# Kernel optimization log

Measured on AMD Instinct MI355X. Metric: run time of the kernel, lower is better.

## Reference

```python
import jax, jax.numpy as jnp
import numpy as np

# DenseCRFParams defaults (kernel bandwidths chosen O(1) since points ~ N(0,1))
GAMMA = 1.0   # spatial kernel bandwidth
ALPHA = 1.0   # bilateral spatial bandwidth
BETA = 1.0    # bilateral feature bandwidth
SPATIAL_KER_WEIGHT = 3.0
BILATERAL_KER_WEIGHT = 5.0
NUM_LABELS = 13
NUM_ITERATIONS = 5
N_POINTS = 8192


def _gauss_kernel(feats):
    # K_ij = exp(-0.5 * ||f_i - f_j||^2), feats: (n, d) -> (n, n)
    sq = jnp.sum(feats * feats, axis=-1)
    d2 = sq[:, None] + sq[None, :] - 2.0 * (feats @ feats.T)
    return jnp.exp(-0.5 * jnp.maximum(d2, 0.0))


def setup_inputs() -> dict:
    key = jax.random.key(0)
    k1, k2 = jax.random.split(key)
    points = jax.random.normal(k1, (N_POINTS, 6), dtype=jnp.float32)
    logits = jax.random.normal(k2, (N_POINTS, NUM_LABELS), dtype=jnp.float32)
    eye = jnp.eye(NUM_LABELS, dtype=jnp.float32)
    return {
        "points": points,
        "logits": logits,
        "spatial_ker_weights": SPATIAL_KER_WEIGHT * eye,
        "bilateral_ker_weights": BILATERAL_KER_WEIGHT * eye,
        "compatibility_matrix": eye,
    }


def reference(points, logits, spatial_ker_weights, bilateral_ker_weights, compatibility_matrix):
    n, num_labels = logits.shape
    xyz = points[:, :3]
    feat = points[:, 3:]

    # Exact Gaussian filtering (the math the permutohedral lattice approximates),
    # normalized by the filter response to all-ones (splat-blur-slice normalization).
    k_spatial = _gauss_kernel(xyz / GAMMA)                                   # (n, n)
    k_bilateral = _gauss_kernel(jnp.concatenate([xyz / ALPHA, feat / BETA], axis=-1))
    norm_s = jnp.sum(k_spatial, axis=1, keepdims=True)                       # (n, 1)
    norm_b = jnp.sum(k_bilateral, axis=1, keepdims=True)

    cur_logits = logits
    for _ in range(NUM_ITERATIONS):
        # NOTE: original uses Softmax(dim=0), i.e. over the point axis — kept faithful.
        q = jax.nn.softmax(cur_logits, axis=0)                               # (n, L)
        spatial_filt = (k_spatial @ q) / norm_s                              # (n, L)
        bilateral_filt = (k_bilateral @ q) / norm_b                          # (n, L)
        # NOTE: original does .view(num_labels, -1) — a raw row-major reshape,
        # NOT a transpose; replicated faithfully with jnp.reshape.
        spatial_out = spatial_ker_weights @ spatial_filt.reshape(num_labels, -1)
        bilateral_out = bilateral_ker_weights @ bilateral_filt.reshape(num_labels, -1)
        msg = compatibility_matrix @ (spatial_out + bilateral_out)           # (L, n)
        cur_logits = msg.reshape(-1, num_labels) + logits                    # (n, L)
    return cur_logits[None]                                                  # (1, n, L)
```

## Files before the change

kernel.cpp:

```cpp
#include <hip/hip_runtime.h>

#define N 8192
#define L 13
#define SEGS 8
#define NSP 32
#define GRID 1024

typedef _Float16 f16x8 __attribute__((ext_vector_type(8)));
typedef _Float16 f16x2 __attribute__((ext_vector_type(2)));
typedef float f32x4 __attribute__((ext_vector_type(4)));
union F16x8U { f16x8 v; f16x2 h[4]; };

#define C1 (-0.72134752044448f)
#define C2 (1.44269504088896f)
#define EBIAS 6.0f

#define SM_NRM  3328
#define SM_SAB  3456
#define SM_M1   5120
#define SM_M2   5289
#define SM_EBUF 5458
#define SMEMW   6290

struct PP {
  const float *points, *logits, *Ws, *Wb, *Cm;
  float *cur, *crd, *snx, *snf, *M1, *M2, *part0, *part1;
  unsigned short *psA, *pbA, *psB, *pbB, *qp0, *qp1, *qp2;
  int *cnt;
};

__device__ __forceinline__ void prep_body(int bid, int t, const PP& P, float* smem) {
  if (bid == 32) {
    if (t < L * L) {
      int r = t / L, c = t % L;
      float a = 0.f, b = 0.f;
      for (int j = 0; j < L; ++j) {
        a += P.Cm[r * L + j] * P.Ws[j * L + c];
        b += P.Cm[r * L + j] * P.Wb[j * L + c];
      }
      P.M1[t] = a; P.M2[t] = b;
    }
    return;
  }
  int p = bid * 256 + t;
  float c6[6];
#pragma unroll
  for (int d = 0; d < 6; ++d) { c6[d] = P.points[p * 6 + d]; P.crd[d * N + p] = c6[d]; }
  float sx = c6[0] * c6[0] + c6[1] * c6[1] + c6[2] * c6[2];
  float sf = c6[3] * c6[3] + c6[4] * c6[4] + c6[5] * c6[5];
  P.snx[p] = sx; P.snf[p] = sf;

  int spair = p >> 5, w = p & 31, rm = w & 15;
  int laneS = (w < 16 ? 0 : 32) + rm;
  int laneB = (w < 16 ? 16 : 48) + rm;
  f16x8 vs = { (_Float16)c6[0], (_Float16)c6[1], (_Float16)c6[2],
               (_Float16)sx, (_Float16)1.0f, (_Float16)0.0f, (_Float16)0.0f, (_Float16)0.0f };
  f16x8 vb = { (_Float16)c6[0], (_Float16)c6[1], (_Float16)c6[2],
               (_Float16)c6[3], (_Float16)c6[4], (_Float16)c6[5],
               (_Float16)(sx + sf), (_Float16)1.0f };
  ((f16x8*)P.qp0, 0);
  ((f16x8*)(P.psA), 0);
  {
    f16x8* a1v = (f16x8*)( (unsigned short*)nullptr == nullptr ? nullptr : nullptr ); (void)a1v;
  }
  extern __device__ int __dummy_never_used;
  (void)__dummy_never_used;
  ((f16x8*)P.pbB, 0);
  struct AA { };
  (void)sizeof(AA);
  f16x8* a1p = (f16x8*)P.cur;
  (void)a1p;
  {
    f16x8* a1 = (f16x8*)P.psB;
    (void)a1;
  }
  {
    unsigned short* a1pack = (unsigned short*)P.qp2 + (size_t)256 * 64 * 8;
    ((f16x8*)a1pack)[(size_t)spair * 64 + laneS] = vs;
    ((f16x8*)a1pack)[(size_t)spair * 64 + laneB] = vb;
  }

  int kc = p >> 5, kk = p & 31;
  int g = (kk < 16) ? (kk >> 2) : ((kk - 16) >> 2);
  int j2 = (kk < 16) ? (kk & 3) : (4 + (kk & 3));
  size_t qb = ((size_t)kc * 64 + g * 16) * 8 + j2;
  unsigned short* qps[3] = {P.qp0, P.qp1, P.qp2};
#pragma unroll
  for (int b = 0; b < 3; ++b) {
    qps[b][qb + 13 * 8] = 0x3C00;
    qps[b][qb + 14 * 8] = 0;
    qps[b][qb + 15 * 8] = 0;
  }

  float (*buf)[256] = (float(*)[256])smem;
#pragma unroll
  for (int l = 0; l < L; ++l) {
    float e = __builtin_amdgcn_exp2f(P.logits[p * L + l] * C2 - EBIAS);
    _Float16 h = (_Float16)e;
    P.qp0[qb + (size_t)l * 8] = *(unsigned short*)&h;
    buf[l][t] = e;
  }
  __syncthreads();
  for (int s = 128; s >= 1; s >>= 1) {
    if (t < s) {
#pragma unroll
      for (int l = 0; l < L; ++l) buf[l][t] += buf[l][t + s];
    }
    __syncthreads();
  }
  if (t < L) P.part0[bid * 16 + t] = buf[t][0];
}

#define PK(dst, va, vb_) { auto _r = __builtin_amdgcn_cvt_pkrtz(va, vb_); dst = *(f16x2*)&_r; }
#define E(x) __builtin_amdgcn_exp2f(x)
#define MFMA16(a_, b_, c_) __builtin_amdgcn_mfma_f32_16x16x32_f16(a_, b_, c_, 0, 0, 0)

__device__ __forceinline__ void filter_body(const PP& P, int bx, int seg, int tid,
                                            const unsigned short* __restrict__ qpin,
                                            unsigned short* __restrict__ psh,
                                            unsigned short* __restrict__ pbh) {
  const unsigned short* a1pack = (const unsigned short*)P.qp2 + (size_t)256 * 64 * 8;
  int lane = tid & 63, wave = tid >> 6;
  int g = lane >> 4, rm = lane & 15;
  int ptile = bx * 64 + wave * 16;
  int p = ptile + rm;

  float x0 = P.crd[p], x1 = P.crd[N + p], x2 = P.crd[2 * N + p];
  float f0 = P.crd[3 * N + p], f1 = P.crd[4 * N + p], f2 = P.crd[5 * N + p];
  float sx = P.snx[p], sf = P.snf[p];

  f16x8 spat = { (_Float16)(C2 * x0), (_Float16)(C2 * x1), (_Float16)(C2 * x2),
                 (_Float16)C1, (_Float16)(C1 * sx),
                 (_Float16)0.0f, (_Float16)0.0f, (_Float16)0.0f };
  f16x8 bil  = { (_Float16)(C2 * x0), (_Float16)(C2 * x1), (_Float16)(C2 * x2),
                 (_Float16)(C2 * f0), (_Float16)(C2 * f1), (_Float16)(C2 * f2),
                 (_Float16)C1, (_Float16)(C1 * (sx + sf)) };
  f16x8 z8 = {0, 0, 0, 0, 0, 0, 0, 0};
  f16x8 Bs0 = (g == 0) ? spat : z8;
  f16x8 Bb0 = (g == 1) ? bil : z8;
  f16x8 Bs1 = (g == 2) ? spat : z8;
  f16x8 Bb1 = (g == 3) ? bil : z8;

  f32x4 acc_s = {0.f, 0.f, 0.f, 0.f};
  f32x4 acc_b = {0.f, 0.f, 0.f, 0.f};
  const f32x4 zero = {0.f, 0.f, 0.f, 0.f};
  const f16x8* a1 = (const f16x8*)a1pack;
  const f16x8* qp = (const f16x8*)qpin;

  int sp0 = seg * NSP;
#pragma unroll 2
  for (int sp = sp0; sp < sp0 + NSP; ++sp) {
    f16x8 A  = a1[(size_t)sp * 64 + lane];
    f16x8 bq = qp[(size_t)sp * 64 + lane];
    f32x4 ax0 = MFMA16(A, Bs0, zero);
    f32x4 ab0 = MFMA16(A, Bb0, zero);
    f32x4 ax1 = MFMA16(A, Bs1, zero);
    f32x4 ab1 = MFMA16(A, Bb1, zero);
    F16x8U us, ub;
    PK(us.h[0], E(ax0[0]), E(ax0[1]));
    PK(us.h[1], E(ax0[2]), E(ax0[3]));
    PK(us.h[2], E(ax1[0]), E(ax1[1]));
    PK(us.h[3], E(ax1[2]), E(ax1[3]));
    PK(ub.h[0], E(ab0[0]), E(ab0[1]));
    PK(ub.h[1], E(ab0[2]), E(ab0[3]));
    PK(ub.h[2], E(ab1[0]), E(ab1[1]));
    PK(ub.h[3], E(ab1[2]), E(ab1[3]));
    acc_s = MFMA16(us.v, bq, acc_s);
    acc_b = MFMA16(ub.v, bq, acc_b);
  }

  int pout = ptile + g * 4;
  size_t base = ((size_t)seg * N + pout) * 16 + rm;
#pragma unroll
  for (int r = 0; r < 4; ++r) {
    _Float16 hs = (_Float16)acc_s[r];
    _Float16 hb = (_Float16)acc_b[r];
    psh[base + (size_t)r * 16] = *(unsigned short*)&hs;
    pbh[base + (size_t)r * 16] = *(unsigned short*)&hb;
  }
}

__device__ __forceinline__ void redmix_body(const PP& P, int bx, int t,
                                            const unsigned short* __restrict__ psh,
                                            const unsigned short* __restrict__ pbh,
                                            const float* __restrict__ partin,
                                            float* __restrict__ partout,
                                            unsigned short* __restrict__ qpout,
                                            int R, int last, float* smem) {
  float (*buf)[256] = (float(*)[256])smem;
  float* nrm = smem + SM_NRM;
  float (*sAB)[64][13] = (float(*)[64][13])(smem + SM_SAB);
  float* m1s = smem + SM_M1;
  float* m2s = smem + SM_M2;
  float* ebuf = smem + SM_EBUF;

#pragma unroll
  for (int l = 0; l < L; ++l) buf[l][t] = (t < R) ? partin[t * 16 + l] : 0.f;
  if (t < 169) { m1s[t] = P.M1[t]; m2s[t] = P.M2[t]; }
  __syncthreads();
  for (int s = 128; s >= 1; s >>= 1) {
    if (t < s) {
#pragma unroll
      for (int l = 0; l < L; ++l) buf[l][t] += buf[l][t + s];
    }
    __syncthreads();
  }

  int pi = t >> 2, src = (t >> 1) & 1, half = t & 1;
  int p = bx * 64 + pi;
  const unsigned short* basep = src ? pbh : psh;
  float a8[8] = {0.f, 0.f, 0.f, 0.f, 0.f, 0.f, 0.f, 0.f};
#pragma unroll
  for (int seg = 0; seg < SEGS; ++seg) {
    f16x8 v = *(const f16x8*)(basep + ((size_t)seg * N + p) * 16 + half * 8);
#pragma unroll
    for (int j = 0; j < 8; ++j) a8[j] += (float)v[j];
  }
  if (half) nrm[pi * 2 + src] = a8[5];
  __syncthreads();
  {
    float inv_norm = 1.0f / nrm[pi * 2 + src];
#pragma unroll
    for (int j = 0; j < 8; ++j) {
      int col = half * 8 + j;
      if (col < L) sAB[src][pi][col] = a8[j] * (1.0f / buf[col][0]) * inv_norm;
    }
  }
  __syncthreads();

  for (int oi = t; oi < 832; oi += 256) {
    int r = oi >> 6, ci = oi & 63;
    float v = 0.f;
#pragma unroll
    for (int j = 0; j < L; ++j) {
      v = fmaf(m1s[r * L + j], sAB[0][ci][j], v);
      v = fmaf(m2s[r * L + j], sAB[1][ci][j], v);
    }
    int i = (r << 13) + bx * 64 + ci;
    float o = v + P.logits[i];
    if (last) {
      P.cur[i] = o;
    } else {
      float e = __builtin_amdgcn_exp2f(o * C2 - EBIAS);
      ebuf[oi] = e;
      unsigned int pr = (unsigned int)i / 13u;
      int l = i - pr * 13;
      int kc = pr >> 5, kk = pr & 31;
      int g = (kk < 16) ? (kk >> 2) : ((kk - 16) >> 2);
      int j2 = (kk < 16) ? (kk & 3) : (4 + (kk & 3));
      _Float16 h = (_Float16)e;
      qpout[((size_t)kc * 64 + g * 16 + l) * 8 + j2] = *(unsigned short*)&h;
    }
  }
  if (last) return;
  __syncthreads();

  if (t < 26) {
    int g = (t >= 13) ? 1 : 0, l = t - g * 13;
    int lo = g * 32, hi = lo + 32;
    float s_ = 0.f;
#pragma unroll
    for (int r = 0; r < L; ++r) {
      int base = ((l - 2 * r - bx * 64) % 13 + 26) % 13;
#pragma unroll
      for (int m = 0; m < 5; ++m) {
        int ci = base + 13 * m;
        if (ci >= lo && ci < hi) s_ += ebuf[r * 64 + ci];
      }
    }
    partout[(2 * bx + g) * 16 + l] = s_;
  }
}

__device__ __forceinline__ void pick_bufs(const PP& P, int it,
                                          const unsigned short*& qpin, unsigned short*& qpout,
                                          unsigned short*& psh, unsigned short*& pbh,
                                          const float*& partin, float*& partout) {
  int qi = it % 3, qo = (it + 1) % 3;
  qpin = qi == 0 ? P.qp0 : qi == 1 ? P.qp1 : P.qp2;
  qpout = qo == 0 ? P.qp0 : qo == 1 ? P.qp1 : P.qp2;
  psh = (it & 1) ? P.psB : P.psA;
  pbh = (it & 1) ? P.pbB : P.pbA;
  partin = (it & 1) ? P.part1 : P.part0;
  partout = (it & 1) ? P.part0 : P.part1;
}

__global__ __launch_bounds__(256) void crf_mega(PP P) {
  __shared__ float smem[SMEMW];
  __shared__ int flag;
  int t = threadIdx.x;
  int bid = blockIdx.x;
  int bx = bid >> 3, seg = bid & 7;
  int* prepcnt = P.cnt;
  int* cnt1 = P.cnt + 1;
  int* cnt2 = P.cnt + 1 + 640;

  if (bid < 33) {
    prep_body(bid, t, P, smem);
    __threadfence();
    __syncthreads();
    if (t == 0) atomicAdd(prepcnt, 1);
  }
  if (t == 0) { while (atomicAdd(prepcnt, 0) < 33) __builtin_amdgcn_s_sleep(8); }
  __syncthreads();
  __threadfence();

  for (int it = 0; it < 5; ++it) {
    const unsigned short* qpin; unsigned short* qpout;
    unsigned short *psh, *pbh;
    const float* partin; float* partout;
    pick_bufs(P, it, qpin, qpout, psh, pbh, partin, partout);
    int R = (it == 0) ? 32 : 256;
    int last = (it == 4);

    if (it >= 1) {
      if (t == 0) { while (atomicAdd(&cnt2[(it - 1) * 8 + seg], 0) < 16) __builtin_amdgcn_s_sleep(2); }
      __syncthreads();
      __threadfence();
    }

    filter_body(P, bx, seg, t, qpin, psh, pbh);
    __threadfence();
    __syncthreads();
    if (t == 0) flag = (atomicAdd(&cnt1[it * 128 + bx], 1) == SEGS - 1) ? 1 : 0;
    __syncthreads();
    if (!flag) continue;

    if (it >= 1) {
      if (t == 0) {
        for (int s = 0; s < 8; ++s)
          while (atomicAdd(&cnt2[(it - 1) * 8 + s], 0) < 16) __builtin_amdgcn_s_sleep(2);
      }
      __syncthreads();
      __threadfence();
    }
    redmix_body(P, bx, t, psh, pbh, partin, partout, qpout, R, last, smem);
    if (!last) {
      __threadfence();
      __syncthreads();
      if (t == 0) atomicAdd(&cnt2[it * 8 + (bx >> 4)], 1);
    }
  }
}

__global__ __launch_bounds__(256) void prep_k(PP P) {
  __shared__ float smem[SMEMW];
  prep_body(blockIdx.x, threadIdx.x, P, smem);
}
__global__ __launch_bounds__(256) void filter_k(PP P, int it) {
  const unsigned short* qpin; unsigned short* qpout;
  unsigned short *psh, *pbh;
  const float* partin; float* partout;
  pick_bufs(P, it, qpin, qpout, psh, pbh, partin, partout);
  filter_body(P, blockIdx.x, blockIdx.y, threadIdx.x, qpin, psh, pbh);
}
__global__ __launch_bounds__(256) void redmix_k(PP P, int it) {
  __shared__ float smem[SMEMW];
  const unsigned short* qpin; unsigned short* qpout;
  unsigned short *psh, *pbh;
  const float* partin; float* partout;
  pick_bufs(P, it, qpin, qpout, psh, pbh, partin, partout);
  redmix_body(P, blockIdx.x, threadIdx.x, psh, pbh, partin, partout, qpout,
              it == 0 ? 32 : 256, it == 4 ? 1 : 0, smem);
}

extern "C" void kernel_launch(void* const* d_in, const int* in_sizes, int n_in,
                              void* d_out, int out_size, void* d_ws, size_t ws_size,
                              hipStream_t stream) {
  PP P;
  P.points = (const float*)d_in[0];
  P.logits = (const float*)d_in[1];
  P.Ws = (const float*)d_in[2];
  P.Wb = (const float*)d_in[3];
  P.Cm = (const float*)d_in[4];
  P.cur = (float*)d_out;

  char* base = (char*)d_ws;
  P.cnt = (int*)base;                         base += 4096;
  float* w = (float*)base;
  P.crd  = w;   w += 6 * N;
  P.snx  = w;   w += N;
  P.snf  = w;   w += N;
  P.M1   = w;   w += 256;
  P.M2   = w;   w += 256;
  P.part0 = w;  w += 256 * 16;
  P.part1 = w;  w += 256 * 16;
  unsigned short* u = (unsigned short*)w;
  P.psA = u;  u += (size_t)SEGS * N * 16;
  P.pbA = u;  u += (size_t)SEGS * N * 16;
  P.psB = u;  u += (size_t)SEGS * N * 16;
  P.pbB = u;  u += (size_t)SEGS * N * 16;
  P.qp0 = u;  u += (size_t)256 * 64 * 8;
  P.qp1 = u;  u += (size_t)256 * 64 * 8;
  P.qp2 = u;  u += (size_t)256 * 64 * 8;
  u += (size_t)256 * 64 * 8;

  (void)hipMemsetAsync(P.cnt, 0, 4096, stream);

  int nb = 0;
  (void)hipOccupancyMaxActiveBlocksPerMultiprocessor(&nb, crf_mega, 256, 0);
  int dev = 0;
  (void)hipGetDevice(&dev);
  hipDeviceProp_t prop{};
  (void)hipGetDeviceProperties(&prop, dev);
  bool coop = ((long)nb * (long)prop.multiProcessorCount >= GRID);

  hipError_t err = hipErrorUnknown;
  if (coop) {
    void* args[] = { &P };
    err = hipLaunchCooperativeKernel((void*)crf_mega, dim3(GRID), dim3(256), args, 0, stream);
  }
  if (!coop || err != hipSuccess) {
    prep_k<<<33, 256, 0, stream>>>(P);
    for (int it = 0; it < 5; ++it) {
      filter_k<<<dim3(128, SEGS), 256, 0, stream>>>(P, it);
      redmix_k<<<128, 256, 0, stream>>>(P, it);
    }
  }
}
```

Measured before the change: 165.5 us.

## Replace cooperative persistent kernel with per-iteration fused filter+reduce launches

Removes the cooperative persistent megakernel and its spin-wait inter-block barriers. It now launches one prep kernel plus five per-iteration kernels, each fusing the filter pass with a last-arriving-block reduction and mix step, so kernel boundaries provide the global sync. Counter zeroing moves into the prep kernel instead of a memset, and the buffers shrink to double-buffered qp and single partial buffers. This trades spin-polling and occupancy constraints for launch overhead, and cross-iteration overlap is lost.

```diff
diff --git a/kernel.cpp b/kernel.cpp
--- a/kernel.cpp
+++ b/kernel.cpp
@@ -4,7 +4,6 @@
 #define L 13
 #define SEGS 8
 #define NSP 32
-#define GRID 1024
 
 typedef _Float16 f16x8 __attribute__((ext_vector_type(8)));
 typedef _Float16 f16x2 __attribute__((ext_vector_type(2)));
@@ -25,12 +24,14 @@
 struct PP {
   const float *points, *logits, *Ws, *Wb, *Cm;
   float *cur, *crd, *snx, *snf, *M1, *M2, *part0, *part1;
-  unsigned short *psA, *pbA, *psB, *pbB, *qp0, *qp1, *qp2;
+  unsigned short *psh, *pbh, *qp0, *qp1, *a1;
   int *cnt;
 };
 
-__device__ __forceinline__ void prep_body(int bid, int t, const PP& P, float* smem) {
-  if (bid == 32) {
+
+__global__ __launch_bounds__(256) void prep_kernel(PP P) {
+  int t = threadIdx.x;
+  if (blockIdx.x == 32) {
     if (t < L * L) {
       int r = t / L, c = t % L;
       float a = 0.f, b = 0.f;
@@ -40,9 +41,10 @@
       }
       P.M1[t] = a; P.M2[t] = b;
     }
+    for (int i = t; i < 5 * 128; i += 256) P.cnt[i] = 0;
     return;
   }
-  int p = bid * 256 + t;
+  int p = blockIdx.x * 256 + t;
   float c6[6];
 #pragma unroll
   for (int d = 0; d < 6; ++d) { c6[d] = P.points[p * 6 + d]; P.crd[d * N + p] = c6[d]; }
@@ -58,41 +60,21 @@
   f16x8 vb = { (_Float16)c6[0], (_Float16)c6[1], (_Float16)c6[2],
                (_Float16)c6[3], (_Float16)c6[4], (_Float16)c6[5],
                (_Float16)(sx + sf), (_Float16)1.0f };
-  ((f16x8*)P.qp0, 0);
-  ((f16x8*)(P.psA), 0);
-  {
-    f16x8* a1v = (f16x8*)( (unsigned short*)nullptr == nullptr ? nullptr : nullptr ); (void)a1v;
-  }
-  extern __device__ int __dummy_never_used;
-  (void)__dummy_never_used;
-  ((f16x8*)P.pbB, 0);
-  struct AA { };
-  (void)sizeof(AA);
-  f16x8* a1p = (f16x8*)P.cur;
-  (void)a1p;
-  {
-    f16x8* a1 = (f16x8*)P.psB;
-    (void)a1;
-  }
-  {
-    unsigned short* a1pack = (unsigned short*)P.qp2 + (size_t)256 * 64 * 8;
-    ((f16x8*)a1pack)[(size_t)spair * 64 + laneS] = vs;
-    ((f16x8*)a1pack)[(size_t)spair * 64 + laneB] = vb;
-  }
+  ((f16x8*)P.a1)[(size_t)spair * 64 + laneS] = vs;
+  ((f16x8*)P.a1)[(size_t)spair * 64 + laneB] = vb;
 
   int kc = p >> 5, kk = p & 31;
   int g = (kk < 16) ? (kk >> 2) : ((kk - 16) >> 2);
   int j2 = (kk < 16) ? (kk & 3) : (4 + (kk & 3));
   size_t qb = ((size_t)kc * 64 + g * 16) * 8 + j2;
-  unsigned short* qps[3] = {P.qp0, P.qp1, P.qp2};
-#pragma unroll
-  for (int b = 0; b < 3; ++b) {
-    qps[b][qb + 13 * 8] = 0x3C00;
-    qps[b][qb + 14 * 8] = 0;
-    qps[b][qb + 15 * 8] = 0;
-  }
-
-  float (*buf)[256] = (float(*)[256])smem;
+  P.qp0[qb + 13 * 8] = 0x3C00;
+  P.qp0[qb + 14 * 8] = 0;
+  P.qp0[qb + 15 * 8] = 0;
+  P.qp1[qb + 13 * 8] = 0x3C00;
+  P.qp1[qb + 14 * 8] = 0;
+  P.qp1[qb + 15 * 8] = 0;
+
+  __shared__ float buf[13][256];
 #pragma unroll
   for (int l = 0; l < L; ++l) {
     float e = __builtin_amdgcn_exp2f(P.logits[p * L + l] * C2 - EBIAS);
@@ -108,81 +90,14 @@
     }
     __syncthreads();
   }
-  if (t < L) P.part0[bid * 16 + t] = buf[t][0];
+  if (t < L) P.part0[blockIdx.x * 16 + t] = buf[t][0];
 }
 
 #define PK(dst, va, vb_) { auto _r = __builtin_amdgcn_cvt_pkrtz(va, vb_); dst = *(f16x2*)&_r; }
 #define E(x) __builtin_amdgcn_exp2f(x)
 #define MFMA16(a_, b_, c_) __builtin_amdgcn_mfma_f32_16x16x32_f16(a_, b_, c_, 0, 0, 0)
 
-__device__ __forceinline__ void filter_body(const PP& P, int bx, int seg, int tid,
-                                            const unsigned short* __restrict__ qpin,
-                                            unsigned short* __restrict__ psh,
-                                            unsigned short* __restrict__ pbh) {
-  const unsigned short* a1pack = (const unsigned short*)P.qp2 + (size_t)256 * 64 * 8;
-  int lane = tid & 63, wave = tid >> 6;
-  int g = lane >> 4, rm = lane & 15;
-  int ptile = bx * 64 + wave * 16;
-  int p = ptile + rm;
-
-  float x0 = P.crd[p], x1 = P.crd[N + p], x2 = P.crd[2 * N + p];
-  float f0 = P.crd[3 * N + p], f1 = P.crd[4 * N + p], f2 = P.crd[5 * N + p];
-  float sx = P.snx[p], sf = P.snf[p];
-
-  f16x8 spat = { (_Float16)(C2 * x0), (_Float16)(C2 * x1), (_Float16)(C2 * x2),
-                 (_Float16)C1, (_Float16)(C1 * sx),
-                 (_Float16)0.0f, (_Float16)0.0f, (_Float16)0.0f };
-  f16x8 bil  = { (_Float16)(C2 * x0), (_Float16)(C2 * x1), (_Float16)(C2 * x2),
-                 (_Float16)(C2 * f0), (_Float16)(C2 * f1), (_Float16)(C2 * f2),
-                 (_Float16)C1, (_Float16)(C1 * (sx + sf)) };
-  f16x8 z8 = {0, 0, 0, 0, 0, 0, 0, 0};
-  f16x8 Bs0 = (g == 0) ? spat : z8;
-  f16x8 Bb0 = (g == 1) ? bil : z8;
-  f16x8 Bs1 = (g == 2) ? spat : z8;
-  f16x8 Bb1 = (g == 3) ? bil : z8;
-
-  f32x4 acc_s = {0.f, 0.f, 0.f, 0.f};
-  f32x4 acc_b = {0.f, 0.f, 0.f, 0.f};
-  const f32x4 zero = {0.f, 0.f, 0.f, 0.f};
-  const f16x8* a1 = (const f16x8*)a1pack;
-  const f16x8* qp = (const f16x8*)qpin;
-
-  int sp0 = seg * NSP;
-#pragma unroll 2
-  for (int sp = sp0; sp < sp0 + NSP; ++sp) {
-    f16x8 A  = a1[(size_t)sp * 64 + lane];
-    f16x8 bq = qp[(size_t)sp * 64 + lane];
-    f32x4 ax0 = MFMA16(A, Bs0, zero);
-    f32x4 ab0 = MFMA16(A, Bb0, zero);
-    f32x4 ax1 = MFMA16(A, Bs1, zero);
-    f32x4 ab1 = MFMA16(A, Bb1, zero);
-    F16x8U us, ub;
-    PK(us.h[0], E(ax0[0]), E(ax0[1]));
-    PK(us.h[1], E(ax0[2]), E(ax0[3]));
-    PK(us.h[2], E(ax1[0]), E(ax1[1]));
-    PK(us.h[3], E(ax1[2]), E(ax1[3]));
-    PK(ub.h[0], E(ab0[0]), E(ab0[1]));
-    PK(ub.h[1], E(ab0[2]), E(ab0[3]));
-    PK(ub.h[2], E(ab1[0]), E(ab1[1]));
-    PK(ub.h[3], E(ab1[2]), E(ab1[3]));
-    acc_s = MFMA16(us.v, bq, acc_s);
-    acc_b = MFMA16(ub.v, bq, acc_b);
-  }
-
-  int pout = ptile + g * 4;
-  size_t base = ((size_t)seg * N + pout) * 16 + rm;
-#pragma unroll
-  for (int r = 0; r < 4; ++r) {
-    _Float16 hs = (_Float16)acc_s[r];
-    _Float16 hb = (_Float16)acc_b[r];
-    psh[base + (size_t)r * 16] = *(unsigned short*)&hs;
-    pbh[base + (size_t)r * 16] = *(unsigned short*)&hb;
-  }
-}
-
 __device__ __forceinline__ void redmix_body(const PP& P, int bx, int t,
-                                            const unsigned short* __restrict__ psh,
-                                            const unsigned short* __restrict__ pbh,
                                             const float* __restrict__ partin,
                                             float* __restrict__ partout,
                                             unsigned short* __restrict__ qpout,
@@ -208,7 +123,7 @@
 
   int pi = t >> 2, src = (t >> 1) & 1, half = t & 1;
   int p = bx * 64 + pi;
-  const unsigned short* basep = src ? pbh : psh;
+  const unsigned short* basep = src ? P.pbh : P.psh;
   float a8[8] = {0.f, 0.f, 0.f, 0.f, 0.f, 0.f, 0.f, 0.f};
 #pragma unroll
   for (int seg = 0; seg < SEGS; ++seg) {
@@ -272,96 +187,88 @@
   }
 }
 
-__device__ __forceinline__ void pick_bufs(const PP& P, int it,
-                                          const unsigned short*& qpin, unsigned short*& qpout,
-                                          unsigned short*& psh, unsigned short*& pbh,
-                                          const float*& partin, float*& partout) {
-  int qi = it % 3, qo = (it + 1) % 3;
-  qpin = qi == 0 ? P.qp0 : qi == 1 ? P.qp1 : P.qp2;
-  qpout = qo == 0 ? P.qp0 : qo == 1 ? P.qp1 : P.qp2;
-  psh = (it & 1) ? P.psB : P.psA;
-  pbh = (it & 1) ? P.pbB : P.pbA;
-  partin = (it & 1) ? P.part1 : P.part0;
-  partout = (it & 1) ? P.part0 : P.part1;
-}
-
-__global__ __launch_bounds__(256) void crf_mega(PP P) {
+__global__ __launch_bounds__(256) void filterfused(PP P, int it) {
   __shared__ float smem[SMEMW];
   __shared__ int flag;
-  int t = threadIdx.x;
-  int bid = blockIdx.x;
-  int bx = bid >> 3, seg = bid & 7;
-  int* prepcnt = P.cnt;
-  int* cnt1 = P.cnt + 1;
-  int* cnt2 = P.cnt + 1 + 640;
-
-  if (bid < 33) {
-    prep_body(bid, t, P, smem);
-    __threadfence();
-    __syncthreads();
-    if (t == 0) atomicAdd(prepcnt, 1);
-  }
-  if (t == 0) { while (atomicAdd(prepcnt, 0) < 33) __builtin_amdgcn_s_sleep(8); }
-  __syncthreads();
+  int tid = threadIdx.x;
+  int bx = blockIdx.x, seg = blockIdx.y;
+
+  const unsigned short* qpin = (it & 1) ? P.qp1 : P.qp0;
+  unsigned short* qpout = (it & 1) ? P.qp0 : P.qp1;
+  const float* partin = (it & 1) ? P.part1 : P.part0;
+  float* partout = (it & 1) ? P.part0 : P.part1;
+  int R = (it == 0) ? 32 : 256;
+  int last = (it == 4);
+
+  {
+    int lane = tid & 63, wave = tid >> 6;
+    int g = lane >> 4, rm = lane & 15;
+    int ptile = bx * 64 + wave * 16;
+    int p = ptile + rm;
+
+    float x0 = P.crd[p], x1 = P.crd[N + p], x2 = P.crd[2 * N + p];
+    float f0 = P.crd[3 * N + p], f1 = P.crd[4 * N + p], f2 = P.crd[5 * N + p];
+    float sx = P.snx[p], sf = P.snf[p];
+
+    f16x8 spat = { (_Float16)(C2 * x0), (_Float16)(C2 * x1), (_Float16)(C2 * x2),
+                   (_Float16)C1, (_Float16)(C1 * sx),
+                   (_Float16)0.0f, (_Float16)0.0f, (_Float16)0.0f };
+    f16x8 bil  = { (_Float16)(C2 * x0), (_Float16)(C2 * x1), (_Float16)(C2 * x2),
+                   (_Float16)(C2 * f0), (_Float16)(C2 * f1), (_Float16)(C2 * f2),
+                   (_Float16)C1, (_Float16)(C1 * (sx + sf)) };
+    f16x8 z8 = {0, 0, 0, 0, 0, 0, 0, 0};
+    f16x8 Bs0 = (g == 0) ? spat : z8;
+    f16x8 Bb0 = (g == 1) ? bil : z8;
+    f16x8 Bs1 = (g == 2) ? spat : z8;
+    f16x8 Bb1 = (g == 3) ? bil : z8;
+
+    f32x4 acc_s = {0.f, 0.f, 0.f, 0.f};
+    f32x4 acc_b = {0.f, 0.f, 0.f, 0.f};
+    const f32x4 zero = {0.f, 0.f, 0.f, 0.f};
+    const f16x8* a1 = (const f16x8*)P.a1;
+    const f16x8* qp = (const f16x8*)qpin;
+
+    int sp0 = seg * NSP;
+#pragma unroll 2
+    for (int sp = sp0; sp < sp0 + NSP; ++sp) {
+      f16x8 A  = a1[(size_t)sp * 64 + lane];
+      f16x8 bq = qp[(size_t)sp * 64 + lane];
+      f32x4 ax0 = MFMA16(A, Bs0, zero);
+      f32x4 ab0 = MFMA16(A, Bb0, zero);
+      f32x4 ax1 = MFMA16(A, Bs1, zero);
+      f32x4 ab1 = MFMA16(A, Bb1, zero);
+      F16x8U us, ub;
+      PK(us.h[0], E(ax0[0]), E(ax0[1]));
+      PK(us.h[1], E(ax0[2]), E(ax0[3]));
+      PK(us.h[2], E(ax1[0]), E(ax1[1]));
+      PK(us.h[3], E(ax1[2]), E(ax1[3]));
+      PK(ub.h[0], E(ab0[0]), E(ab0[1]));
+      PK(ub.h[1], E(ab0[2]), E(ab0[3]));
+      PK(ub.h[2], E(ab1[0]), E(ab1[1]));
+      PK(ub.h[3], E(ab1[2]), E(ab1[3]));
+      acc_s = MFMA16(us.v, bq, acc_s);
+      acc_b = MFMA16(ub.v, bq, acc_b);
+    }
+
+    int pout = ptile + g * 4;
+    size_t base = ((size_t)seg * N + pout) * 16 + rm;
+#pragma unroll
+    for (int r = 0; r < 4; ++r) {
+      _Float16 hs = (_Float16)acc_s[r];
+      _Float16 hb = (_Float16)acc_b[r];
+      P.psh[base + (size_t)r * 16] = *(unsigned short*)&hs;
+      P.pbh[base + (size_t)r * 16] = *(unsigned short*)&hb;
+    }
+  }
+
   __threadfence();
-
-  for (int it = 0; it < 5; ++it) {
-    const unsigned short* qpin; unsigned short* qpout;
-    unsigned short *psh, *pbh;
-    const float* partin; float* partout;
-    pick_bufs(P, it, qpin, qpout, psh, pbh, partin, partout);
-    int R = (it == 0) ? 32 : 256;
-    int last = (it == 4);
-
-    if (it >= 1) {
-      if (t == 0) { while (atomicAdd(&cnt2[(it - 1) * 8 + seg], 0) < 16) __builtin_amdgcn_s_sleep(2); }
-      __syncthreads();
-      __threadfence();
-    }
-
-    filter_body(P, bx, seg, t, qpin, psh, pbh);
-    __threadfence();
-    __syncthreads();
-    if (t == 0) flag = (atomicAdd(&cnt1[it * 128 + bx], 1) == SEGS - 1) ? 1 : 0;
-    __syncthreads();
-    if (!flag) continue;
-
-    if (it >= 1) {
-      if (t == 0) {
-        for (int s = 0; s < 8; ++s)
-          while (atomicAdd(&cnt2[(it - 1) * 8 + s], 0) < 16) __builtin_amdgcn_s_sleep(2);
-      }
-      __syncthreads();
-      __threadfence();
-    }
-    redmix_body(P, bx, t, psh, pbh, partin, partout, qpout, R, last, smem);
-    if (!last) {
-      __threadfence();
-      __syncthreads();
-      if (t == 0) atomicAdd(&cnt2[it * 8 + (bx >> 4)], 1);
-    }
-  }
-}
-
-__global__ __launch_bounds__(256) void prep_k(PP P) {
-  __shared__ float smem[SMEMW];
-  prep_body(blockIdx.x, threadIdx.x, P, smem);
-}
-__global__ __launch_bounds__(256) void filter_k(PP P, int it) {
-  const unsigned short* qpin; unsigned short* qpout;
-  unsigned short *psh, *pbh;
-  const float* partin; float* partout;
-  pick_bufs(P, it, qpin, qpout, psh, pbh, partin, partout);
-  filter_body(P, blockIdx.x, blockIdx.y, threadIdx.x, qpin, psh, pbh);
-}
-__global__ __launch_bounds__(256) void redmix_k(PP P, int it) {
-  __shared__ float smem[SMEMW];
-  const unsigned short* qpin; unsigned short* qpout;
-  unsigned short *psh, *pbh;
-  const float* partin; float* partout;
-  pick_bufs(P, it, qpin, qpout, psh, pbh, partin, partout);
-  redmix_body(P, blockIdx.x, threadIdx.x, psh, pbh, partin, partout, qpout,
-              it == 0 ? 32 : 256, it == 4 ? 1 : 0, smem);
+  __syncthreads();
+  if (tid == 0) flag = (atomicAdd(&P.cnt[it * 128 + bx], 1) == SEGS - 1) ? 1 : 0;
+  __syncthreads();
+  if (!flag) return;
+  __threadfence();
+
+  redmix_body(P, bx, tid, partin, partout, qpout, R, last, smem);
 }
 
 extern "C" void kernel_launch(void* const* d_in, const int* in_sizes, int n_in,
@@ -376,7 +283,7 @@
   P.cur = (float*)d_out;
 
   char* base = (char*)d_ws;
-  P.cnt = (int*)base;                         base += 4096;
+  P.cnt = (int*)base;  base += 4096;
   float* w = (float*)base;
   P.crd  = w;   w += 6 * N;
   P.snx  = w;   w += N;
@@ -386,35 +293,13 @@
   P.part0 = w;  w += 256 * 16;
   P.part1 = w;  w += 256 * 16;
   unsigned short* u = (unsigned short*)w;
-  P.psA = u;  u += (size_t)SEGS * N * 16;
-  P.pbA = u;  u += (size_t)SEGS * N * 16;
-  P.psB = u;  u += (size_t)SEGS * N * 16;
-  P.pbB = u;  u += (size_t)SEGS * N * 16;
+  P.psh = u;  u += (size_t)SEGS * N * 16;
+  P.pbh = u;  u += (size_t)SEGS * N * 16;
   P.qp0 = u;  u += (size_t)256 * 64 * 8;
   P.qp1 = u;  u += (size_t)256 * 64 * 8;
-  P.qp2 = u;  u += (size_t)256 * 64 * 8;
-  u += (size_t)256 * 64 * 8;
-
-  (void)hipMemsetAsync(P.cnt, 0, 4096, stream);
-
-  int nb = 0;
-  (void)hipOccupancyMaxActiveBlocksPerMultiprocessor(&nb, crf_mega, 256, 0);
-  int dev = 0;
-  (void)hipGetDevice(&dev);
-  hipDeviceProp_t prop{};
-  (void)hipGetDeviceProperties(&prop, dev);
-  bool coop = ((long)nb * (long)prop.multiProcessorCount >= GRID);
-
-  hipError_t err = hipErrorUnknown;
-  if (coop) {
-    void* args[] = { &P };
-    err = hipLaunchCooperativeKernel((void*)crf_mega, dim3(GRID), dim3(256), args, 0, stream);
-  }
-  if (!coop || err != hipSuccess) {
-    prep_k<<<33, 256, 0, stream>>>(P);
-    for (int it = 0; it < 5; ++it) {
-      filter_k<<<dim3(128, SEGS), 256, 0, stream>>>(P, it);
-      redmix_k<<<128, 256, 0, stream>>>(P, it);
-    }
-  }
+  P.a1  = u;  u += (size_t)256 * 64 * 8;
+
+  prep_kernel<<<33, 256, 0, stream>>>(P);
+  for (int it = 0; it < 5; ++it)
+    filterfused<<<dim3(N / 64, SEGS), 256, 0, stream>>>(P, it);
 }
```

Measured after the change: 640.0 us. +286.8%, slower.
